# Optimization experiments

Measured on AMD Instinct MI355X. Metric: run time of the kernel, lower is better.

## Reference

```python
import jax, jax.numpy as jnp
import numpy as np
from jax.ops import segment_sum

NUM_GRAPHS = 64


def _leaky_relu(x):
    return jnp.where(x >= 0, x, 0.01 * x)


def setup_inputs() -> dict:
    key = jax.random.key(0)
    ks = jax.random.split(key, 8)
    N, E, D = 100000, 1600000, 128
    x = jax.random.normal(ks[0], (N, D), dtype=jnp.float32)
    edge_index = jax.random.randint(ks[1], (2, E), 0, N, dtype=jnp.int64)
    batch = jnp.sort(jax.random.randint(ks[2], (N,), 0, NUM_GRAPHS, dtype=jnp.int64))
    s = 1.0 / np.sqrt(D)
    W1 = jax.random.normal(ks[3], (D, D), dtype=jnp.float32) * s
    b1 = jnp.zeros((D,), dtype=jnp.float32)
    W2 = jax.random.normal(ks[4], (D, D), dtype=jnp.float32) * s
    b2 = jnp.zeros((D,), dtype=jnp.float32)
    fcW = jax.random.normal(ks[5], (D, 1), dtype=jnp.float32) * s
    fcb = jnp.zeros((1,), dtype=jnp.float32)
    return {"x": x, "edge_index": edge_index, "batch": batch,
            "W1": W1, "b1": b1, "W2": W2, "b2": b2, "fcW": fcW, "fcb": fcb}


def reference(x, edge_index, batch, W1, b1, W2, b2, fcW, fcb):
    N = x.shape[0]
    # GCNConv: add self-loops, symmetric normalization D^-1/2 A D^-1/2
    loop = jnp.arange(N, dtype=edge_index.dtype)
    row = jnp.concatenate([edge_index[0], loop])  # source j
    col = jnp.concatenate([edge_index[1], loop])  # target i
    deg = segment_sum(jnp.ones_like(col, dtype=x.dtype), col, num_segments=N)
    dis = jax.lax.rsqrt(deg)  # deg >= 1 due to self-loops
    norm = dis[row] * dis[col]  # [E+N]

    def conv(h, W, b):
        h = h @ W                               # [N, D'] linear transform
        msg = h[row] * norm[:, None]            # gather + scale
        agg = segment_sum(msg, col, num_segments=N)  # scatter-add
        return agg + b

    h = _leaky_relu(conv(x, W1, b1))
    h = _leaky_relu(conv(h, W2, b2))

    # global_mean_pool over batch ids
    sums = segment_sum(h, batch, num_segments=NUM_GRAPHS)
    cnts = segment_sum(jnp.ones((N,), dtype=h.dtype), batch, num_segments=NUM_GRAPHS)
    pooled = sums / jnp.maximum(cnts, 1.0)[:, None]
    return pooled @ fcW + fcb  # [NUM_GRAPHS, 1]
```

## Files before the change

### kernel.cpp

```cpp
#include <hip/hip_runtime.h>
#include <hip/hip_bf16.h>
#include <math.h>

#define D 128
#define NUM_GRAPHS 64
#define CHUNK 8192
#define BUCK_SH 8
#define BUCK_N 256
#define BCAP 8192
#define PSLICE 8
#define HROW 136

typedef __bf16 bf16x8 __attribute__((ext_vector_type(8)));
typedef __bf16 bf16x2 __attribute__((ext_vector_type(2)));
typedef float f32x4 __attribute__((ext_vector_type(4)));
typedef float f32x2 __attribute__((ext_vector_type(2)));

__device__ inline unsigned char f32_to_fp8(float x) {
    int pk = __builtin_amdgcn_cvt_pk_fp8_f32(x, x, 0, false);
    return (unsigned char)(pk & 0xff);
}
__device__ inline f32x2 fp8x2_to_f32(unsigned short us) {
    return __builtin_amdgcn_cvt_pk_f32_fp8((unsigned int)us, false);
}

__global__ void k_prepW(const float* __restrict__ Wa, const float* __restrict__ Wb,
                        __bf16* __restrict__ WfA, __bf16* __restrict__ WfB,
                        float* __restrict__ pooled,
                        int* __restrict__ gcur,
                        const int* __restrict__ batch, int* __restrict__ gstart, int N) {
    int gid = blockIdx.x * 256 + threadIdx.x;
    if (gid < NUM_GRAPHS * D) pooled[gid] = 0.f;
    if (gid < 512) gcur[gid] = 0;
    if (gid >= 16384 && gid <= 16384 + NUM_GRAPHS) {
        int g = gid - 16384;
        int lo = 0, hi = N;
        while (lo < hi) { int mid = (lo + hi) >> 1; if (batch[mid] < g) lo = mid + 1; else hi = mid; }
        gstart[g] = lo;
    }
    if (gid >= 32768) return;
    const float* W = (gid < 16384) ? Wa : Wb;
    __bf16* Wf = (gid < 16384) ? WfA : WfB;
    int idx = gid & 16383;
    int j = idx & 7, lane = (idx >> 3) & 63, kc = (idx >> 9) & 3, ft = idx >> 11;
    int k = kc * 32 + (lane >> 4) * 8 + j;
    int f = ft * 16 + (lane & 15);
    Wf[idx] = (__bf16)W[k * D + f];
}

template <typename T>
__device__ __forceinline__ void gemm_body(int bid, int tid, const T* __restrict__ X,
                                          const __bf16* __restrict__ Wfrag,
                                          unsigned char* __restrict__ Y8, int N) {
    int w = tid >> 6, lane = tid & 63;
    int quad = lane >> 4, m = lane & 15;
    int nodeA = bid * 64 + w * 16 + m;
    if (nodeA >= N) nodeA = N - 1;

    bf16x8 a[4];
#pragma unroll
    for (int kc = 0; kc < 4; kc++) {
        int kb = kc * 32 + quad * 8;
        if constexpr (sizeof(T) == 4) {
            f32x4 x0 = *(const f32x4*)(X + (size_t)nodeA * D + kb);
            f32x4 x1 = *(const f32x4*)(X + (size_t)nodeA * D + kb + 4);
#pragma unroll
            for (int j = 0; j < 4; j++) { a[kc][j] = (__bf16)x0[j]; a[kc][4 + j] = (__bf16)x1[j]; }
        } else {
            a[kc] = *(const bf16x8*)(X + (size_t)nodeA * D + kb);
        }
    }

    f32x4 d[8];
#pragma unroll
    for (int ft = 0; ft < 8; ft++) {
        d[ft] = (f32x4){0.f, 0.f, 0.f, 0.f};
#pragma unroll
        for (int kc = 0; kc < 4; kc++) {
            bf16x8 b = *(const bf16x8*)(Wfrag + (((ft << 2) | kc) * 64 + lane) * 8);
            d[ft] = __builtin_amdgcn_mfma_f32_16x16x32_bf16(a[kc], b, d[ft], 0, 0, 0);
        }
    }

#pragma unroll
    for (int r = 0; r < 4; r++) {
        int node = bid * 64 + w * 16 + quad * 4 + r;
        if (node < N) {
#pragma unroll
            for (int ft = 0; ft < 8; ft++)
                Y8[(size_t)node * D + ft * 16 + m] = f32_to_fp8(d[ft][r]);
        }
    }
}

__launch_bounds__(256)
__global__ void k_bin_gemm(const int* __restrict__ ei, int* __restrict__ gcur,
                           int* __restrict__ bbuf, int nbuck, int E, int nchunk,
                           const float* __restrict__ X, const __bf16* __restrict__ Wfrag,
                           unsigned char* __restrict__ Y8, int N) {
    __shared__ int h[512];
    __shared__ int base[512];

    if (blockIdx.x >= nchunk) {
        gemm_body<float>(blockIdx.x - nchunk, threadIdx.x, X, Wfrag, Y8, N);
        return;
    }

    int tid = threadIdx.x;
    for (int b = tid; b < nbuck; b += 256) h[b] = 0;
    __syncthreads();
    int lo = blockIdx.x * CHUNK;
    if (lo + CHUNK <= E) {
        const int4* c4 = (const int4*)(ei + E + lo);
#pragma unroll 2
        for (int i = tid; i < CHUNK / 4; i += 256) {
            int4 c = c4[i];
            atomicAdd(&h[c.x >> BUCK_SH], 1);
            atomicAdd(&h[c.y >> BUCK_SH], 1);
            atomicAdd(&h[c.z >> BUCK_SH], 1);
            atomicAdd(&h[c.w >> BUCK_SH], 1);
        }
    } else {
        for (int i = tid; i < CHUNK; i += 256) {
            int e = lo + i;
            if (e < E) atomicAdd(&h[ei[E + e] >> BUCK_SH], 1);
        }
    }
    __syncthreads();
    for (int b = tid; b < nbuck; b += 256) {
        base[b] = atomicAdd(&gcur[b], h[b]);
        h[b] = 0;
    }
    __syncthreads();
    if (lo + CHUNK <= E) {
        const int4* r4 = (const int4*)(ei + lo);
        const int4* c4 = (const int4*)(ei + E + lo);
#pragma unroll 2
        for (int i = tid; i < CHUNK / 4; i += 256) {
            int4 r = r4[i];
            int4 c = c4[i];
            int rr[4] = {r.x, r.y, r.z, r.w};
            int cc[4] = {c.x, c.y, c.z, c.w};
#pragma unroll
            for (int u = 0; u < 4; u++) {
                int b = cc[u] >> BUCK_SH;
                int pos = base[b] + atomicAdd(&h[b], 1);
                if (pos < BCAP) bbuf[(size_t)b * BCAP + pos] = rr[u] | ((cc[u] & (BUCK_N - 1)) << 17);
            }
        }
    } else {
        for (int i = tid; i < CHUNK; i += 256) {
            int e = lo + i;
            if (e < E) {
                int r = ei[e], c = ei[E + e];
                int b = c >> BUCK_SH;
                int pos = base[b] + atomicAdd(&h[b], 1);
                if (pos < BCAP) bbuf[(size_t)b * BCAP + pos] = r | ((c & (BUCK_N - 1)) << 17);
            }
        }
    }
}

__global__ void k_place(const int* __restrict__ bbuf, const int* __restrict__ gcur,
                        int* __restrict__ esrc,
                        int* __restrict__ cnt, int* __restrict__ offs,
                        float* __restrict__ dis, int N) {
    __shared__ int h[256];
    __shared__ int sc[256];
    __shared__ int cur[256];
    int b = blockIdx.x, tid = threadIdx.x;
    int start = b * BCAP;
    int count = gcur[b]; if (count > BCAP) count = BCAP;
    int end = start + count;
    h[tid] = 0;
    __syncthreads();
    for (int i = start + tid; i < end; i += 256) atomicAdd(&h[(bbuf[i] >> 17) & 255], 1);
    __syncthreads();
    int local = h[tid];
    sc[tid] = local;
    __syncthreads();
    for (int off = 1; off < 256; off <<= 1) {
        int xv = (tid >= off) ? sc[tid - off] : 0;
        __syncthreads();
        sc[tid] += xv;
        __syncthreads();
    }
    int excl = sc[tid] - local;
    cur[tid] = start + excl;
    int c = b * 256 + tid;
    if (c < N) {
        cnt[c]  = local;
        offs[c] = start + excl;
        dis[c]  = rsqrtf(1.0f + (float)local);
    }
    __syncthreads();
    for (int i = start + tid; i < end; i += 256) {
        int p = bbuf[i];
        int pos = atomicAdd(&cur[(p >> 17) & 255], 1);
        esrc[pos] = p & 0x1FFFF;
    }
}

__launch_bounds__(256)
__global__ void k_agg_gemm(const unsigned char* __restrict__ Hs8,
                           const int* __restrict__ offs, const int* __restrict__ cnt,
                           const float* __restrict__ dis, const int* __restrict__ esrc,
                           const float* __restrict__ bias,
                           const __bf16* __restrict__ Wfrag,
                           unsigned char* __restrict__ Y8, int N) {
    __shared__ __bf16 hl[32 * HROW];
    int tid = threadIdx.x;
    int w = tid >> 6, lane = tid & 63;
    int node0 = blockIdx.x * 32 + w * 8;
    float b0 = bias[lane * 2], b1v = bias[lane * 2 + 1];

    for (int nn = 0; nn < 8; nn++) {
        int node = node0 + nn;
        if (node < N) {
            int start = offs[node];
            int len = cnt[node];
            float di = dis[node];
            f32x2 h = fp8x2_to_f32(*(const unsigned short*)(Hs8 + (size_t)node * D + lane * 2));
            float acc0 = h[0] * di;
            float acc1 = h[1] * di;

            for (int k0 = 0; k0 < len; k0 += 64) {
                int mm = len - k0; if (mm > 64) mm = 64;
                int ep = esrc[start + k0 + (lane < mm ? lane : 0)];
                float dvl = dis[ep];
                int j = 0;
                for (; j + 16 <= mm; j += 16) {
                    int s[16]; float dv[16]; unsigned short hv[16];
#pragma unroll
                    for (int u = 0; u < 16; u++) { s[u] = __shfl(ep, j + u); dv[u] = __shfl(dvl, j + u); }
#pragma unroll
                    for (int u = 0; u < 16; u++) hv[u] = *(const unsigned short*)(Hs8 + (size_t)s[u] * D + lane * 2);
#pragma unroll
                    for (int u = 0; u < 16; u++) { f32x2 f = fp8x2_to_f32(hv[u]); acc0 += f[0] * dv[u]; acc1 += f[1] * dv[u]; }
                }
                for (; j + 4 <= mm; j += 4) {
                    int s[4]; float dv[4]; unsigned short hv[4];
#pragma unroll
                    for (int u = 0; u < 4; u++) { s[u] = __shfl(ep, j + u); dv[u] = __shfl(dvl, j + u); }
#pragma unroll
                    for (int u = 0; u < 4; u++) hv[u] = *(const unsigned short*)(Hs8 + (size_t)s[u] * D + lane * 2);
#pragma unroll
                    for (int u = 0; u < 4; u++) { f32x2 f = fp8x2_to_f32(hv[u]); acc0 += f[0] * dv[u]; acc1 += f[1] * dv[u]; }
                }
                for (; j < mm; j++) {
                    int s = __shfl(ep, j);
                    float dv = __shfl(dvl, j);
                    f32x2 f = fp8x2_to_f32(*(const unsigned short*)(Hs8 + (size_t)s * D + lane * 2));
                    acc0 += f[0] * dv; acc1 += f[1] * dv;
                }
            }

            acc0 = acc0 * di + b0;
            acc1 = acc1 * di + b1v;
            acc0 = acc0 >= 0.f ? acc0 : 0.01f * acc0;
            acc1 = acc1 >= 0.f ? acc1 : 0.01f * acc1;
            bf16x2 o; o[0] = (__bf16)acc0; o[1] = (__bf16)acc1;
            *(bf16x2*)&hl[(w * 8 + nn) * HROW + lane * 2] = o;
        } else {
            bf16x2 z; z[0] = (__bf16)0.f; z[1] = (__bf16)0.f;
            *(bf16x2*)&hl[(w * 8 + nn) * HROW + lane * 2] = z;
        }
    }
    __syncthreads();

    int quad = lane >> 4, m = lane & 15;
    int rtile = w & 1, fthalf = w >> 1;
    int lrow = rtile * 16 + m;
    bf16x8 a[4];
#pragma unroll
    for (int kc = 0; kc < 4; kc++)
        a[kc] = *(const bf16x8*)&hl[lrow * HROW + kc * 32 + quad * 8];

    int nb = blockIdx.x * 32 + rtile * 16 + quad * 4;
    float scv[4];
#pragma unroll
    for (int r = 0; r < 4; r++) scv[r] = (nb + r < N) ? dis[nb + r] : 0.f;

#pragma unroll
    for (int ft = 0; ft < 4; ft++) {
        int gft = fthalf * 4 + ft;
        f32x4 dacc = (f32x4){0.f, 0.f, 0.f, 0.f};
#pragma unroll
        for (int kc = 0; kc < 4; kc++) {
            bf16x8 b = *(const bf16x8*)(Wfrag + (((gft << 2) | kc) * 64 + lane) * 8);
            dacc = __builtin_amdgcn_mfma_f32_16x16x32_bf16(a[kc], b, dacc, 0, 0, 0);
        }
#pragma unroll
        for (int r = 0; r < 4; r++) {
            int node = nb + r;
            if (node < N)
                Y8[(size_t)node * D + gft * 16 + m] = f32_to_fp8(dacc[r] * scv[r]);
        }
    }
}

__launch_bounds__(256)
__global__ void k_agg(const unsigned char* __restrict__ Hs8, __bf16* __restrict__ O,
                      const int* __restrict__ offs, const int* __restrict__ cnt,
                      const float* __restrict__ dis, const int* __restrict__ esrc,
                      const float* __restrict__ bias, int N) {
    int wave = (blockIdx.x * 256 + threadIdx.x) >> 6;
    int lane = threadIdx.x & 63;
    int node0 = wave * 8;
    float b0 = bias[lane * 2], b1 = bias[lane * 2 + 1];

    for (int nn = 0; nn < 8; nn++) {
        int node = node0 + nn;
        if (node >= N) return;
        int start = offs[node];
        int len = cnt[node];
        float di = dis[node];
        f32x2 h = fp8x2_to_f32(*(const unsigned short*)(Hs8 + (size_t)node * D + lane * 2));
        float acc0 = h[0];
        float acc1 = h[1];

        for (int k0 = 0; k0 < len; k0 += 64) {
            int mm = len - k0; if (mm > 64) mm = 64;
            int ep = esrc[start + k0 + (lane < mm ? lane : 0)];
            int j = 0;
            for (; j + 16 <= mm; j += 16) {
                int s[16]; unsigned short hv[16];
#pragma unroll
                for (int u = 0; u < 16; u++) s[u] = __shfl(ep, j + u);
#pragma unroll
                for (int u = 0; u < 16; u++) hv[u] = *(const unsigned short*)(Hs8 + (size_t)s[u] * D + lane * 2);
#pragma unroll
                for (int u = 0; u < 16; u++) { f32x2 f = fp8x2_to_f32(hv[u]); acc0 += f[0]; acc1 += f[1]; }
            }
            for (; j + 4 <= mm; j += 4) {
                int s[4]; unsigned short hv[4];
#pragma unroll
                for (int u = 0; u < 4; u++) s[u] = __shfl(ep, j + u);
#pragma unroll
                for (int u = 0; u < 4; u++) hv[u] = *(const unsigned short*)(Hs8 + (size_t)s[u] * D + lane * 2);
#pragma unroll
                for (int u = 0; u < 4; u++) { f32x2 f = fp8x2_to_f32(hv[u]); acc0 += f[0]; acc1 += f[1]; }
            }
            for (; j < mm; j++) {
                int s = __shfl(ep, j);
                f32x2 f = fp8x2_to_f32(*(const unsigned short*)(Hs8 + (size_t)s * D + lane * 2));
                acc0 += f[0]; acc1 += f[1];
            }
        }

        acc0 = acc0 * di + b0;
        acc1 = acc1 * di + b1;
        acc0 = acc0 >= 0.f ? acc0 : 0.01f * acc0;
        acc1 = acc1 >= 0.f ? acc1 : 0.01f * acc1;
        bf16x2 o; o[0] = (__bf16)acc0; o[1] = (__bf16)acc1;
        *(bf16x2*)(O + (size_t)node * D + lane * 2) = o;
    }
}

__launch_bounds__(256)
__global__ void k_pool(const __bf16* __restrict__ H, const int* __restrict__ gstart,
                       float* __restrict__ pooled) {
    __shared__ float sdata[256 * 9];
    int g = blockIdx.x / PSLICE;
    int slice = blockIdx.x - g * PSLICE;
    int gs = gstart[g], ge = gstart[g + 1];
    int cg = ge - gs;
    int r0 = gs + (int)((long long)cg * slice / PSLICE);
    int r1 = gs + (int)((long long)cg * (slice + 1) / PSLICE);
    int t = threadIdx.x;
    int rg = t >> 4, fb = t & 15;

    float acc[8];
#pragma unroll
    for (int j = 0; j < 8; j++) acc[j] = 0.f;
    for (int r = r0 + rg; r < r1; r += 16) {
        bf16x8 v = *(const bf16x8*)(H + (size_t)r * D + fb * 8);
#pragma unroll
        for (int j = 0; j < 8; j++) acc[j] += (float)v[j];
    }
#pragma unroll
    for (int j = 0; j < 8; j++) sdata[t * 9 + j] = acc[j];
    __syncthreads();
#pragma unroll
    for (int s = 128; s >= 16; s >>= 1) {
        if (t < s) {
#pragma unroll
            for (int j = 0; j < 8; j++) sdata[t * 9 + j] += sdata[(t + s) * 9 + j];
        }
        __syncthreads();
    }
    if (t < 16) {
#pragma unroll
        for (int j = 0; j < 8; j++) atomicAdd(&pooled[g * D + t * 8 + j], sdata[t * 9 + j]);
    }
}

__launch_bounds__(64)
__global__ void k_fc(const float* __restrict__ pooled, const int* __restrict__ gstart,
                     const float* __restrict__ fcW, const float* __restrict__ fcb,
                     float* __restrict__ out) {
    int t = threadIdx.x;
    float s = 0.f;
#pragma unroll 8
    for (int k = 0; k < D; k += 4) {
        f32x4 pv = *(const f32x4*)(pooled + t * D + k);
        f32x4 wv = *(const f32x4*)(fcW + k);
        s += pv[0] * wv[0] + pv[1] * wv[1] + pv[2] * wv[2] + pv[3] * wv[3];
    }
    float c = (float)(gstart[t + 1] - gstart[t]);
    out[t] = s / fmaxf(c, 1.0f) + fcb[0];
}

extern "C" void kernel_launch(void* const* d_in, const int* in_sizes, int n_in,
                              void* d_out, int out_size, void* d_ws, size_t ws_size,
                              hipStream_t stream) {
    const float* x    = (const float*)d_in[0];
    const int*   ei   = (const int*)d_in[1];
    const int*   batch= (const int*)d_in[2];
    const float* W1   = (const float*)d_in[3];
    const float* b1   = (const float*)d_in[4];
    const float* W2   = (const float*)d_in[5];
    const float* b2   = (const float*)d_in[6];
    const float* fcW  = (const float*)d_in[7];
    const float* fcb  = (const float*)d_in[8];
    float* out = (float*)d_out;

    int N = in_sizes[0] / D;
    int E = in_sizes[1] / 2;

    int NBUCK  = (N + BUCK_N - 1) >> BUCK_SH;
    int NCHUNK = (E + CHUNK - 1) / CHUNK;

    char* p = (char*)d_ws;
    auto alloc = [&](size_t bytes) { char* r = p; p += (bytes + 255) & ~(size_t)255; return r; };
    int*    cnt    = (int*)   alloc((size_t)N * 4);
    int*    offs   = (int*)   alloc((size_t)N * 4);
    float*  dis    = (float*) alloc((size_t)N * 4);
    int*    gcur   = (int*)   alloc(512 * 4);
    int*    bbuf   = (int*)   alloc((size_t)NBUCK * BCAP * 4);
    int*    esrc   = (int*)   alloc((size_t)NBUCK * BCAP * 4);
    unsigned char* bufA8 = (unsigned char*)alloc((size_t)N * D);
    unsigned char* bufC8 = (unsigned char*)alloc((size_t)N * D);
    __bf16* bufB   = (__bf16*)alloc((size_t)N * D * 2);
    __bf16* Wf1    = (__bf16*)alloc((size_t)D * D * 2);
    __bf16* Wf2    = (__bf16*)alloc((size_t)D * D * 2);
    float*  pooled = (float*) alloc((size_t)NUM_GRAPHS * D * 4);
    int*    gstart = (int*)   alloc((NUM_GRAPHS + 1) * 4);

    int gblocks = (N + 63) / 64;
    int ablocks = (N + 31) / 32;

    k_prepW<<<129, 256, 0, stream>>>(W1, W2, Wf1, Wf2, pooled, gcur, batch, gstart, N);

    k_bin_gemm<<<NCHUNK + gblocks, 256, 0, stream>>>(ei, gcur, bbuf, NBUCK, E, NCHUNK,
                                                     x, Wf1, bufA8, N);
    k_place<<<NBUCK, 256, 0, stream>>>(bbuf, gcur, esrc, cnt, offs, dis, N);

    k_agg_gemm<<<ablocks, 256, 0, stream>>>(bufA8, offs, cnt, dis, esrc, b1, Wf2, bufC8, N);

    k_agg<<<ablocks, 256, 0, stream>>>(bufC8, bufB, offs, cnt, dis, esrc, b2, N);

    k_pool<<<NUM_GRAPHS * PSLICE, 256, 0, stream>>>(bufB, gstart, pooled);
    k_fc<<<1, 64, 0, stream>>>(pooled, gstart, fcW, fcb, out);
}
```

Before: 292.1 us.

## Prescale layer-1 features by degree norm in k_place and fuse fc into pool

After building the CSR buckets, k_place rescales each fp8 row of the first-layer transformed features by its own inverse-sqrt degree. This lets the layer-1 aggregation skip the per-edge dis gather, shuffle and multiply, matching the layer-2 path. It also removes the separate k_fc launch: the last k_pool block, detected with an atomic counter, computes the final linear layer. The cost is an extra read-modify-write pass over the fp8 feature buffer with a second fp8 rounding. The buffer is padded to a whole number of buckets so that pass stays in bounds.

```diff
diff --git a/kernel.cpp b/kernel.cpp
--- a/kernel.cpp
+++ b/kernel.cpp
@@ -20,17 +20,22 @@
     int pk = __builtin_amdgcn_cvt_pk_fp8_f32(x, x, 0, false);
     return (unsigned char)(pk & 0xff);
 }
-__device__ inline f32x2 fp8x2_to_f32(unsigned short us) {
+template <bool HI>
+__device__ inline f32x2 fp8x2_to_f32(unsigned int us) {
+    return __builtin_amdgcn_cvt_pk_f32_fp8(us, HI);
+}
+__device__ inline f32x2 fp8x2_to_f32_us(unsigned short us) {
     return __builtin_amdgcn_cvt_pk_f32_fp8((unsigned int)us, false);
 }
 
 __global__ void k_prepW(const float* __restrict__ Wa, const float* __restrict__ Wb,
                         __bf16* __restrict__ WfA, __bf16* __restrict__ WfB,
-                        float* __restrict__ pooled,
+                        float* __restrict__ pooled, int* __restrict__ done,
                         int* __restrict__ gcur,
                         const int* __restrict__ batch, int* __restrict__ gstart, int N) {
     int gid = blockIdx.x * 256 + threadIdx.x;
     if (gid < NUM_GRAPHS * D) pooled[gid] = 0.f;
+    if (gid == 0) *done = 0;
     if (gid < 512) gcur[gid] = 0;
     if (gid >= 16384 && gid <= 16384 + NUM_GRAPHS) {
         int g = gid - 16384;
@@ -164,10 +169,11 @@
 __global__ void k_place(const int* __restrict__ bbuf, const int* __restrict__ gcur,
                         int* __restrict__ esrc,
                         int* __restrict__ cnt, int* __restrict__ offs,
-                        float* __restrict__ dis, int N) {
+                        float* __restrict__ dis, unsigned char* __restrict__ z1, int N) {
     __shared__ int h[256];
     __shared__ int sc[256];
     __shared__ int cur[256];
+    __shared__ float sdis[256];
     int b = blockIdx.x, tid = threadIdx.x;
     int start = b * BCAP;
     int count = gcur[b]; if (count > BCAP) count = BCAP;
@@ -188,16 +194,30 @@
     int excl = sc[tid] - local;
     cur[tid] = start + excl;
     int c = b * 256 + tid;
+    float dv = rsqrtf(1.0f + (float)local);
+    sdis[tid] = dv;
     if (c < N) {
         cnt[c]  = local;
         offs[c] = start + excl;
-        dis[c]  = rsqrtf(1.0f + (float)local);
+        dis[c]  = dv;
     }
     __syncthreads();
     for (int i = start + tid; i < end; i += 256) {
         int p = bbuf[i];
         int pos = atomicAdd(&cur[(p >> 17) & 255], 1);
         esrc[pos] = p & 0x1FFFF;
+    }
+    int nrows = N - b * 256; if (nrows > 256) nrows = 256; if (nrows < 0) nrows = 0;
+    unsigned int* zp = (unsigned int*)(z1 + (size_t)b * 256 * D);
+    for (int i = tid; i < nrows * 32; i += 256) {
+        int row = i >> 5;
+        float s = sdis[row];
+        unsigned int v = zp[i];
+        f32x2 lo = fp8x2_to_f32<false>(v);
+        f32x2 hi = fp8x2_to_f32<true>(v);
+        unsigned int u = (unsigned int)__builtin_amdgcn_cvt_pk_fp8_f32(lo[0] * s, lo[1] * s, 0, false);
+        u = (unsigned int)__builtin_amdgcn_cvt_pk_fp8_f32(hi[0] * s, hi[1] * s, (int)u, true);
+        zp[i] = u;
     }
 }
 
@@ -220,38 +240,36 @@
             int start = offs[node];
             int len = cnt[node];
             float di = dis[node];
-            f32x2 h = fp8x2_to_f32(*(const unsigned short*)(Hs8 + (size_t)node * D + lane * 2));
-            float acc0 = h[0] * di;
-            float acc1 = h[1] * di;
+            f32x2 h = fp8x2_to_f32_us(*(const unsigned short*)(Hs8 + (size_t)node * D + lane * 2));
+            float acc0 = h[0];
+            float acc1 = h[1];
 
             for (int k0 = 0; k0 < len; k0 += 64) {
                 int mm = len - k0; if (mm > 64) mm = 64;
                 int ep = esrc[start + k0 + (lane < mm ? lane : 0)];
-                float dvl = dis[ep];
                 int j = 0;
                 for (; j + 16 <= mm; j += 16) {
-                    int s[16]; float dv[16]; unsigned short hv[16];
-#pragma unroll
-                    for (int u = 0; u < 16; u++) { s[u] = __shfl(ep, j + u); dv[u] = __shfl(dvl, j + u); }
+                    int s[16]; unsigned short hv[16];
+#pragma unroll
+                    for (int u = 0; u < 16; u++) s[u] = __shfl(ep, j + u);
 #pragma unroll
                     for (int u = 0; u < 16; u++) hv[u] = *(const unsigned short*)(Hs8 + (size_t)s[u] * D + lane * 2);
 #pragma unroll
-                    for (int u = 0; u < 16; u++) { f32x2 f = fp8x2_to_f32(hv[u]); acc0 += f[0] * dv[u]; acc1 += f[1] * dv[u]; }
+                    for (int u = 0; u < 16; u++) { f32x2 f = fp8x2_to_f32_us(hv[u]); acc0 += f[0]; acc1 += f[1]; }
                 }
                 for (; j + 4 <= mm; j += 4) {
-                    int s[4]; float dv[4]; unsigned short hv[4];
-#pragma unroll
-                    for (int u = 0; u < 4; u++) { s[u] = __shfl(ep, j + u); dv[u] = __shfl(dvl, j + u); }
+                    int s[4]; unsigned short hv[4];
+#pragma unroll
+                    for (int u = 0; u < 4; u++) s[u] = __shfl(ep, j + u);
 #pragma unroll
                     for (int u = 0; u < 4; u++) hv[u] = *(const unsigned short*)(Hs8 + (size_t)s[u] * D + lane * 2);
 #pragma unroll
-                    for (int u = 0; u < 4; u++) { f32x2 f = fp8x2_to_f32(hv[u]); acc0 += f[0] * dv[u]; acc1 += f[1] * dv[u]; }
+                    for (int u = 0; u < 4; u++) { f32x2 f = fp8x2_to_f32_us(hv[u]); acc0 += f[0]; acc1 += f[1]; }
                 }
                 for (; j < mm; j++) {
                     int s = __shfl(ep, j);
-                    float dv = __shfl(dvl, j);
-                    f32x2 f = fp8x2_to_f32(*(const unsigned short*)(Hs8 + (size_t)s * D + lane * 2));
-                    acc0 += f[0] * dv; acc1 += f[1] * dv;
+                    f32x2 f = fp8x2_to_f32_us(*(const unsigned short*)(Hs8 + (size_t)s * D + lane * 2));
+                    acc0 += f[0]; acc1 += f[1];
                 }
             }
 
@@ -315,7 +333,7 @@
         int start = offs[node];
         int len = cnt[node];
         float di = dis[node];
-        f32x2 h = fp8x2_to_f32(*(const unsigned short*)(Hs8 + (size_t)node * D + lane * 2));
+        f32x2 h = fp8x2_to_f32_us(*(const unsigned short*)(Hs8 + (size_t)node * D + lane * 2));
         float acc0 = h[0];
         float acc1 = h[1];
 
@@ -330,7 +348,7 @@
 #pragma unroll
                 for (int u = 0; u < 16; u++) hv[u] = *(const unsigned short*)(Hs8 + (size_t)s[u] * D + lane * 2);
 #pragma unroll
-                for (int u = 0; u < 16; u++) { f32x2 f = fp8x2_to_f32(hv[u]); acc0 += f[0]; acc1 += f[1]; }
+                for (int u = 0; u < 16; u++) { f32x2 f = fp8x2_to_f32_us(hv[u]); acc0 += f[0]; acc1 += f[1]; }
             }
             for (; j + 4 <= mm; j += 4) {
                 int s[4]; unsigned short hv[4];
@@ -339,11 +357,11 @@
 #pragma unroll
                 for (int u = 0; u < 4; u++) hv[u] = *(const unsigned short*)(Hs8 + (size_t)s[u] * D + lane * 2);
 #pragma unroll
-                for (int u = 0; u < 4; u++) { f32x2 f = fp8x2_to_f32(hv[u]); acc0 += f[0]; acc1 += f[1]; }
+                for (int u = 0; u < 4; u++) { f32x2 f = fp8x2_to_f32_us(hv[u]); acc0 += f[0]; acc1 += f[1]; }
             }
             for (; j < mm; j++) {
                 int s = __shfl(ep, j);
-                f32x2 f = fp8x2_to_f32(*(const unsigned short*)(Hs8 + (size_t)s * D + lane * 2));
+                f32x2 f = fp8x2_to_f32_us(*(const unsigned short*)(Hs8 + (size_t)s * D + lane * 2));
                 acc0 += f[0]; acc1 += f[1];
             }
         }
@@ -359,8 +377,11 @@
 
 __launch_bounds__(256)
 __global__ void k_pool(const __bf16* __restrict__ H, const int* __restrict__ gstart,
-                       float* __restrict__ pooled) {
+                       float* __restrict__ pooled,
+                       const float* __restrict__ fcW, const float* __restrict__ fcb,
+                       float* __restrict__ out, int* __restrict__ done) {
     __shared__ float sdata[256 * 9];
+    __shared__ int lastflag;
     int g = blockIdx.x / PSLICE;
     int slice = blockIdx.x - g * PSLICE;
     int gs = gstart[g], ge = gstart[g + 1];
@@ -393,22 +414,20 @@
 #pragma unroll
         for (int j = 0; j < 8; j++) atomicAdd(&pooled[g * D + t * 8 + j], sdata[t * 9 + j]);
     }
-}
-
-__launch_bounds__(64)
-__global__ void k_fc(const float* __restrict__ pooled, const int* __restrict__ gstart,
-                     const float* __restrict__ fcW, const float* __restrict__ fcb,
-                     float* __restrict__ out) {
-    int t = threadIdx.x;
-    float s = 0.f;
-#pragma unroll 8
-    for (int k = 0; k < D; k += 4) {
-        f32x4 pv = *(const f32x4*)(pooled + t * D + k);
-        f32x4 wv = *(const f32x4*)(fcW + k);
-        s += pv[0] * wv[0] + pv[1] * wv[1] + pv[2] * wv[2] + pv[3] * wv[3];
-    }
-    float c = (float)(gstart[t + 1] - gstart[t]);
-    out[t] = s / fmaxf(c, 1.0f) + fcb[0];
+    __threadfence();
+    __syncthreads();
+    if (t == 0) lastflag = (atomicAdd(done, 1) == (int)gridDim.x - 1) ? 1 : 0;
+    __syncthreads();
+    if (lastflag) {
+        __threadfence();
+        if (t < NUM_GRAPHS) {
+            float s = 0.f;
+#pragma unroll 4
+            for (int k = 0; k < D; k++) s += pooled[t * D + k] * fcW[k];
+            float c = (float)(gstart[t + 1] - gstart[t]);
+            out[t] = s / fmaxf(c, 1.0f) + fcb[0];
+        }
+    }
 }
 
 extern "C" void kernel_launch(void* const* d_in, const int* in_sizes, int n_in,
@@ -439,27 +458,27 @@
     int*    gcur   = (int*)   alloc(512 * 4);
     int*    bbuf   = (int*)   alloc((size_t)NBUCK * BCAP * 4);
     int*    esrc   = (int*)   alloc((size_t)NBUCK * BCAP * 4);
-    unsigned char* bufA8 = (unsigned char*)alloc((size_t)N * D);
+    unsigned char* bufA8 = (unsigned char*)alloc((size_t)(NBUCK * BUCK_N) * D);
     unsigned char* bufC8 = (unsigned char*)alloc((size_t)N * D);
     __bf16* bufB   = (__bf16*)alloc((size_t)N * D * 2);
     __bf16* Wf1    = (__bf16*)alloc((size_t)D * D * 2);
     __bf16* Wf2    = (__bf16*)alloc((size_t)D * D * 2);
     float*  pooled = (float*) alloc((size_t)NUM_GRAPHS * D * 4);
     int*    gstart = (int*)   alloc((NUM_GRAPHS + 1) * 4);
+    int*    done   = (int*)   alloc(256);
 
     int gblocks = (N + 63) / 64;
     int ablocks = (N + 31) / 32;
 
-    k_prepW<<<129, 256, 0, stream>>>(W1, W2, Wf1, Wf2, pooled, gcur, batch, gstart, N);
+    k_prepW<<<129, 256, 0, stream>>>(W1, W2, Wf1, Wf2, pooled, done, gcur, batch, gstart, N);
 
     k_bin_gemm<<<NCHUNK + gblocks, 256, 0, stream>>>(ei, gcur, bbuf, NBUCK, E, NCHUNK,
                                                      x, Wf1, bufA8, N);
-    k_place<<<NBUCK, 256, 0, stream>>>(bbuf, gcur, esrc, cnt, offs, dis, N);
+    k_place<<<NBUCK, 256, 0, stream>>>(bbuf, gcur, esrc, cnt, offs, dis, bufA8, N);
 
     k_agg_gemm<<<ablocks, 256, 0, stream>>>(bufA8, offs, cnt, dis, esrc, b1, Wf2, bufC8, N);
 
     k_agg<<<ablocks, 256, 0, stream>>>(bufC8, bufB, offs, cnt, dis, esrc, b2, N);
 
-    k_pool<<<NUM_GRAPHS * PSLICE, 256, 0, stream>>>(bufB, gstart, pooled);
-    k_fc<<<1, 64, 0, stream>>>(pooled, gstart, fcW, fcb, out);
-}
+    k_pool<<<NUM_GRAPHS * PSLICE, 256, 0, stream>>>(bufB, gstart, pooled, fcW, fcb, out, done);
+}
```

Measured after the change: 313.1 us. 1.07x slower.
